# Kernel optimization log

Measured on AMD Instinct MI355X. Metric: run time of the kernel, lower is better.

Reference implementation:

```python
import jax, jax.numpy as jnp
import numpy as np

N_REV, N_USER, N_ITEM, DEG, D = 100000, 4096, 4096, 16, 64
HID = 128

def setup_inputs() -> dict:
    key = jax.random.key(0)
    ks = jax.random.split(key, 9)
    return {
        "review_vecs": jax.random.normal(ks[0], (N_REV, D), jnp.float32),
        "user_vecs": jax.random.normal(ks[1], (N_USER, D), jnp.float32),
        "item_vecs": jax.random.normal(ks[2], (N_ITEM, D), jnp.float32),
        "user_weights": jax.random.normal(ks[3], (DEG * 2 * D, HID), jnp.float32) * 0.05,
        "item_weights": jax.random.normal(ks[4], (DEG * 2 * D, HID), jnp.float32) * 0.05,
        "adj0": jax.random.randint(ks[5], (N_USER, DEG), 0, N_REV, jnp.int32),
        "adj1": jax.random.randint(ks[6], (N_USER, DEG), 0, N_ITEM, jnp.int32),
        "adj2": jax.random.randint(ks[7], (N_ITEM, DEG), 0, N_REV, jnp.int32),
        "adj3": jax.random.randint(ks[8], (N_ITEM, DEG), 0, N_USER, jnp.int32),
    }

def _sdpa(q, k, v):
    # dense scaled dot-product attention: q,k [N,d], v [N,F]
    scale = 1.0 / jnp.sqrt(jnp.asarray(q.shape[-1], q.dtype))
    w = jax.nn.softmax(jnp.einsum('nd,md->nm', q, k) * scale, axis=-1)
    return jnp.einsum('nm,mf->nf', w, v)

def reference(review_vecs, user_vecs, item_vecs, user_weights, item_weights,
              adj0, adj1, adj2, adj3):
    # dropout=0.0 -> identity; feature-dim shuffle is random augmentation,
    # replaced by identity permutation for a deterministic reference.
    ur = review_vecs[adj0]           # [Nu, deg, D]
    ri = item_vecs[adj1]             # [Nu, deg, D]
    ir = review_vecs[adj2]           # [Ni, deg, D]
    ru = user_vecs[adj3]             # [Ni, deg, D]
    cu = jnp.concatenate([ur, ri], axis=2).reshape(adj0.shape[0], -1)  # [Nu, deg*2D]
    ci = jnp.concatenate([ir, ru], axis=2).reshape(adj2.shape[0], -1)  # [Ni, deg*2D]
    cu = _sdpa(user_vecs, user_vecs, cu)
    ci = _sdpa(item_vecs, item_vecs, ci)
    user_out = jax.nn.relu(cu @ user_weights)   # [Nu, HID]
    item_out = jax.nn.relu(ci @ item_weights)   # [Ni, HID]
    return user_out, item_out
```

## Files before the change

### kernel.cpp

```cpp
#include <hip/hip_runtime.h>
#include <hip/hip_bf16.h>
#include <math.h>

#define N_NODES 4096
#define N_REV 100000
#define DEG 16
#define DIM 64
#define HID 128

typedef __attribute__((ext_vector_type(8))) short bf16x8;
typedef __attribute__((ext_vector_type(4))) float f32x4;
typedef __attribute__((ext_vector_type(16))) float f32x16;

static __device__ __forceinline__ unsigned pk2(float a, float b) {
    __hip_bfloat162 h = __float22bfloat162_rn(make_float2(a, b));
    return *reinterpret_cast<unsigned*>(&h);
}

static __device__ __forceinline__ void gl_lds16(const void* g, void* l) {
    __builtin_amdgcn_global_load_lds(
        (const __attribute__((address_space(1))) unsigned int*)g,
        (__attribute__((address_space(3))) unsigned int*)l, 16, 0, 0);
}

__global__ __launch_bounds__(256)
void prep_w(const float* __restrict__ uW, const float* __restrict__ iW,
            ushort* __restrict__ wt)
{
    __shared__ float wt_f[64 * 128];
    const int t = threadIdx.x;
    const int side = blockIdx.x >> 5, kc = blockIdx.x & 31;
    const float* __restrict__ W = side ? iW : uW;
    const float4* src = (const float4*)(W + (size_t)kc * 64 * 128);
    #pragma unroll
    for (int j = 0; j < 8; ++j)
        ((float4*)wt_f)[j * 256 + t] = src[j * 256 + t];
    __syncthreads();
    #pragma unroll
    for (int j = 0; j < 4; ++j) {
        int c = j * 256 + t;
        int h = c >> 3, seg = c & 7;
        int sp = seg ^ (h & 7);
        float v[8];
        #pragma unroll
        for (int jj = 0; jj < 8; ++jj) v[jj] = wt_f[(sp * 8 + jj) * 128 + h];
        uint4 o;
        o.x = pk2(v[0], v[1]); o.y = pk2(v[2], v[3]);
        o.z = pk2(v[4], v[5]); o.w = pk2(v[6], v[7]);
        *(uint4*)(wt + ((size_t)(side * 32 + kc) * 1024 + c) * 8) = o;
    }
}

#define GB_STRIDE 16384
#define GADJ_OFF  32768

__global__ __launch_bounds__(256)
void gemm_gather(const float* __restrict__ review,
                 const float* __restrict__ userv,
                 const float* __restrict__ itemv,
                 const ushort* __restrict__ wt,
                 const int* __restrict__ adj0, const int* __restrict__ adj1,
                 const int* __restrict__ adj2, const int* __restrict__ adj3,
                 ushort* __restrict__ vprojT,
                 ushort* __restrict__ Ub, ushort* __restrict__ Ib)
{
    const int t = threadIdx.x;
    if (blockIdx.x >= 512) {
        int i = (blockIdx.x - 512) * 256 + t;
        const float* src; ushort* dst; int j;
        if (i < 32768) { src = userv; dst = Ub; j = i; }
        else           { src = itemv; dst = Ib; j = i - 32768; }
        float4 a = ((const float4*)src)[j * 2];
        float4 b = ((const float4*)src)[j * 2 + 1];
        uint4 o;
        o.x = pk2(a.x, a.y); o.y = pk2(a.z, a.w);
        o.z = pk2(b.x, b.y); o.w = pk2(b.z, b.w);
        ((uint4*)dst)[j] = o;
        return;
    }

    const int side = blockIdx.x >> 8, rem = blockIdx.x & 255;
    const int tile = (rem & 7) | ((rem >> 4) << 3);
    const int hb   = (rem >> 3) & 1;
    const int* __restrict__ adjA = side ? adj2 : adj0;
    const int* __restrict__ adjB = side ? adj3 : adj1;
    const float* __restrict__ vecB = side ? userv : itemv;
    const ushort* __restrict__ wbase = wt + (size_t)side * 32 * 8192;
    ushort* __restrict__ outT = vprojT + (size_t)side * HID * N_NODES;

    __shared__ __align__(16) char smem[36864];
    int* adjs = (int*)(smem + GADJ_OFF);
    const int w = t >> 6, lane = t & 63;
    const int wm = w >> 1, wn = w & 1;
    const int g = lane >> 4, qi = lane & 15;
    const int swz = (qi & 7) << 4;

    if (t < 128)
        ((int4*)adjs)[t] = ((const int4*)(adjA + tile * 512))[t];
    else
        ((int4*)adjs)[t] = ((const int4*)(adjB + tile * 512))[t - 128];
    __syncthreads();

    f32x4 acc[2];
    #pragma unroll
    for (int i = 0; i < 2; ++i) acc[i] = f32x4{0.f, 0.f, 0.f, 0.f};

    auto stage = [&](int kc, int b) {
        const int d = kc >> 1, half = kc & 1;
        char* base = smem + b * GB_STRIDE;
        const float* vs = half ? vecB : review;
        #pragma unroll
        for (int j = 0; j < 2; ++j) {
            int c = j * 256 + t;
            int row = c >> 4, seg = c & 15;
            int idx = adjs[half * 512 + row * 16 + d];
            gl_lds16(vs + (size_t)idx * 64 + (seg ^ (row & 7)) * 4,
                     base + (c >> 6) * 1024);
        }
        const ushort* wsrc = wbase + (size_t)kc * 8192;
        #pragma unroll
        for (int j = 0; j < 2; ++j) {
            int c = j * 256 + t;
            gl_lds16(wsrc + (size_t)(hb * 512 + c) * 8,
                     base + 8192 + (c >> 6) * 1024);
        }
    };

    stage(0, 0);
    __syncthreads();

    for (int kc = 0; kc < 32; ++kc) {
        const int cur = kc & 1;
        if (kc < 31) stage(kc + 1, cur ^ 1);

        const char* cb = smem + cur * GB_STRIDE;
        const int ab0 = (wm * 16 + qi) * 256 + g * 32;
        f32x4 af0 = *(const f32x4*)(cb + ((ab0)       ^ swz));
        f32x4 af1 = *(const f32x4*)(cb + ((ab0 + 16)  ^ swz));
        f32x4 af2 = *(const f32x4*)(cb + ((ab0 + 128) ^ swz));
        f32x4 af3 = *(const f32x4*)(cb + ((ab0 + 144) ^ swz));
        union { unsigned u[4]; bf16x8 s; } A0, A1;
        A0.u[0] = pk2(af0[0], af0[1]); A0.u[1] = pk2(af0[2], af0[3]);
        A0.u[2] = pk2(af1[0], af1[1]); A0.u[3] = pk2(af1[2], af1[3]);
        A1.u[0] = pk2(af2[0], af2[1]); A1.u[1] = pk2(af2[2], af2[3]);
        A1.u[2] = pk2(af3[0], af3[1]); A1.u[3] = pk2(af3[2], af3[3]);

        #pragma unroll
        for (int nf = 0; nf < 2; ++nf) {
            int bbase = 8192 + (wn * 32 + nf * 16 + qi) * 128 + g * 16;
            bf16x8 b0 = *(const bf16x8*)(cb + ((bbase)      ^ swz));
            bf16x8 b1 = *(const bf16x8*)(cb + ((bbase + 64) ^ swz));
            acc[nf] = __builtin_amdgcn_mfma_f32_16x16x32_bf16(A0.s, b0, acc[nf], 0, 0, 0);
            acc[nf] = __builtin_amdgcn_mfma_f32_16x16x32_bf16(A1.s, b1, acc[nf], 0, 0, 0);
        }
        __syncthreads();
    }

    #pragma unroll
    for (int nf = 0; nf < 2; ++nf) {
        int h = hb * 64 + wn * 32 + nf * 16 + qi;
        uint2 p;
        p.x = pk2(acc[nf][0], acc[nf][1]);
        p.y = pk2(acc[nf][2], acc[nf][3]);
        *(uint2*)(outT + (size_t)h * N_NODES + tile * 32 + wm * 16 + g * 4) = p;
    }
}

#define FSTRIDE 24576
#define QSCALE 0.180336880f

__global__ __launch_bounds__(256, 2)
void flash_attn_mfma(const float* __restrict__ userv,
                     const float* __restrict__ itemv,
                     const ushort* __restrict__ Ub,
                     const ushort* __restrict__ Ib,
                     const ushort* __restrict__ vprojT,
                     ushort* __restrict__ po,
                     float* __restrict__ pl)
{
    const int grp  = blockIdx.x & 7;
    const int side = grp >> 2;
    const int qg   = grp & 3;
    const int hi   = blockIdx.x >> 3;
    const int qhi  = hi >> 3;
    const int kvb  = hi & 7;
    const int qb   = qhi * 4 + qg;
    const float* __restrict__ X = side ? itemv : userv;
    const ushort* __restrict__ Xb = side ? Ib : Ub;
    const ushort* __restrict__ V = vprojT + (size_t)side * HID * N_NODES;
    const int part = side * 8 + kvb;

    __shared__ __align__(16) char smem[49152];

    const int t = threadIdx.x;
    const int w = t >> 6, lane = t & 63;
    const int col = lane & 31, h5 = lane >> 5;
    const int q0 = qb * 128 + w * 32;

    bf16x8 qf[4];
    {
        const float* qp = X + (size_t)(q0 + col) * DIM;
        #pragma unroll
        for (int ks = 0; ks < 4; ++ks) {
            int d0 = ks * 16 + h5 * 8;
            float4 v0 = *(const float4*)(qp + d0);
            float4 v1 = *(const float4*)(qp + d0 + 4);
            union { unsigned u[4]; bf16x8 s; } rr;
            rr.u[0] = pk2(v0.x * QSCALE, v0.y * QSCALE);
            rr.u[1] = pk2(v0.z * QSCALE, v0.w * QSCALE);
            rr.u[2] = pk2(v1.x * QSCALE, v1.y * QSCALE);
            rr.u[3] = pk2(v1.z * QSCALE, v1.w * QSCALE);
            qf[ks] = rr.s;
        }
    }

    const f32x16 z16 = {0.f,0.f,0.f,0.f, 0.f,0.f,0.f,0.f,
                        0.f,0.f,0.f,0.f, 0.f,0.f,0.f,0.f};
    f32x16 o[4];
    #pragma unroll
    for (int ht = 0; ht < 4; ++ht) o[ht] = z16;
    float psum = 0.f;

    auto stage = [&](int it, int b) {
        const int k0 = kvb * 512 + it * 64;
        char* base = smem + b * FSTRIDE;
        #pragma unroll
        for (int j = 0; j < 2; ++j) {
            int c = j * 256 + t;
            int row = c >> 3, seg = c & 7;
            gl_lds16(Xb + (size_t)(k0 + row) * 64 + (seg ^ (row & 7)) * 8,
                     base + (c >> 6) * 1024);
        }
        #pragma unroll
        for (int j = 0; j < 4; ++j) {
            int c = j * 256 + t;
            int hh = c >> 3, seg = c & 7;
            gl_lds16(V + (size_t)hh * N_NODES + k0 + (seg ^ (hh & 7)) * 8,
                     base + 8192 + (c >> 6) * 1024);
        }
    };

    stage(0, 0);
    __syncthreads();

    for (int it = 0; it < 8; ++it) {
        const int cur = it & 1;
        if (it < 7) stage(it + 1, cur ^ 1);
        const char* kb = smem + cur * FSTRIDE;
        const char* vt = kb + 8192;

        #pragma unroll
        for (int T = 0; T < 2; ++T) {
            f32x16 s = z16;
            #pragma unroll
            for (int ks = 0; ks < 4; ++ks) {
                int row = T * 32 + col;
                int abase = (row * 128 + ks * 32 + h5 * 16) ^ ((row & 7) << 4);
                bf16x8 ka = *(const bf16x8*)(kb + abase);
                s = __builtin_amdgcn_mfma_f32_32x32x16_bf16(ka, qf[ks], s, 0, 0, 0);
            }
            float p[16];
            #pragma unroll
            for (int r = 0; r < 16; ++r) {
                p[r] = exp2f(s[r]);
                psum += p[r];
            }
            #pragma unroll
            for (int win = 0; win < 2; ++win) {
                unsigned ca0 = pk2(p[win*8 + 0], p[win*8 + 1]);
                unsigned ca1 = pk2(p[win*8 + 2], p[win*8 + 3]);
                unsigned cb0 = pk2(p[win*8 + 4], p[win*8 + 5]);
                unsigned cb1 = pk2(p[win*8 + 6], p[win*8 + 7]);
                asm volatile("v_permlane32_swap_b32 %0, %1"
                             : "+v"(ca0), "+v"(cb0));
                asm volatile("v_permlane32_swap_b32 %0, %1"
                             : "+v"(ca1), "+v"(cb1));
                union { unsigned u[4]; bf16x8 s8; } pa;
                pa.u[0] = ca0; pa.u[1] = ca1; pa.u[2] = cb0; pa.u[3] = cb1;
                #pragma unroll
                for (int ht = 0; ht < 4; ++ht) {
                    int hrow = ht * 32 + col;
                    int vbase = (hrow * 128 + T * 64 + win * 32 + h5 * 16)
                                ^ ((hrow & 7) << 4);
                    bf16x8 vb = *(const bf16x8*)(vt + vbase);
                    o[ht] = __builtin_amdgcn_mfma_f32_32x32x16_bf16(pa.s8, vb, o[ht], 0, 0, 0);
                }
            }
        }
        __syncthreads();
    }

    float pt = psum + __shfl_xor(psum, 32);
    if (lane < 32)
        pl[(size_t)part * N_NODES + q0 + col] = pt;

    ushort* pob = po + (size_t)part * N_NODES * HID;
    #pragma unroll
    for (int ht = 0; ht < 4; ++ht)
        #pragma unroll
        for (int r = 0; r < 16; ++r) {
            int q = q0 + (r & 3) + 8 * (r >> 2) + 4 * h5;
            pob[(size_t)q * HID + ht * 32 + col] =
                (ushort)(pk2(o[ht][r], 0.f) & 0xffffu);
        }
}

__global__ __launch_bounds__(256)
void merge_parts(const ushort* __restrict__ po, const float* __restrict__ pl,
                 float* __restrict__ out)
{
    const int grp  = blockIdx.x & 7;
    const int side = grp >> 2;
    const int qg   = grp & 3;
    const int hi   = blockIdx.x >> 3;
    const int qhi  = hi >> 3;
    const int u    = hi & 7;
    const int t = threadIdx.x;
    const int lidx = u * 256 + t;
    const int q  = (qhi * 4 + qg) * 128 + (lidx >> 4);
    const int h8 = lidx & 15;

    float s[8] = {0.f,0.f,0.f,0.f,0.f,0.f,0.f,0.f};
    float l = 0.f;
    #pragma unroll
    for (int p = 0; p < 8; ++p) {
        int part = side * 8 + p;
        uint4 v = *(const uint4*)(po + (size_t)part * (N_NODES * HID)
                                     + (size_t)q * HID + h8 * 8);
        unsigned uu[4] = {v.x, v.y, v.z, v.w};
        #pragma unroll
        for (int k = 0; k < 4; ++k) {
            union { unsigned u; float f; } lo, hi2;
            lo.u = uu[k] << 16; hi2.u = uu[k] & 0xffff0000u;
            s[k * 2]     += lo.f;
            s[k * 2 + 1] += hi2.f;
        }
        l += pl[(size_t)part * N_NODES + q];
    }
    float li = 1.0f / l;
    float4 r0, r1;
    r0.x = fmaxf(s[0] * li, 0.f); r0.y = fmaxf(s[1] * li, 0.f);
    r0.z = fmaxf(s[2] * li, 0.f); r0.w = fmaxf(s[3] * li, 0.f);
    r1.x = fmaxf(s[4] * li, 0.f); r1.y = fmaxf(s[5] * li, 0.f);
    r1.z = fmaxf(s[6] * li, 0.f); r1.w = fmaxf(s[7] * li, 0.f);
    float* op = out + ((size_t)side * N_NODES + q) * HID + h8 * 8;
    *(float4*)op = r0;
    *(float4*)(op + 4) = r1;
}

extern "C" void kernel_launch(void* const* d_in, const int* in_sizes, int n_in,
                              void* d_out, int out_size, void* d_ws, size_t ws_size,
                              hipStream_t stream)
{
    const float* review = (const float*)d_in[0];
    const float* userv  = (const float*)d_in[1];
    const float* itemv  = (const float*)d_in[2];
    const float* uW     = (const float*)d_in[3];
    const float* iW     = (const float*)d_in[4];
    const int*   adj0   = (const int*)d_in[5];
    const int*   adj1   = (const int*)d_in[6];
    const int*   adj2   = (const int*)d_in[7];
    const int*   adj3   = (const int*)d_in[8];
    float* out = (float*)d_out;

    char* ws = (char*)d_ws;
    float*  pl     = (float*)(ws + 0x000000);
    ushort* wt     = (ushort*)(ws + 0x080000);
    ushort* vprojT = (ushort*)(ws + 0x180000);
    ushort* Ub     = (ushort*)(ws + 0x380000);
    ushort* Ib     = (ushort*)(ws + 0x400000);
    ushort* po     = (ushort*)(ws + 0x480000);

    prep_w<<<64, 256, 0, stream>>>(uW, iW, wt);
    gemm_gather<<<768, 256, 0, stream>>>(review, userv, itemv, wt,
                                         adj0, adj1, adj2, adj3, vprojT,
                                         Ub, Ib);
    flash_attn_mfma<<<512, 256, 0, stream>>>(userv, itemv, Ub, Ib, vprojT,
                                             po, pl);
    merge_parts<<<512, 256, 0, stream>>>(po, pl, out);
}
```

Baseline: 56.45 us.

## Fuse all four stages into one cooperative persistent kernel with grid syncs

Replaces the four separate launches (weight prep, gather-GEMM, flash attention, merge) with a single cooperative kernel of 256 blocks of 512 threads. Each block runs two 256-thread units and separates the stages with grid-wide barriers. The aim is to remove per-launch overhead and inter-kernel gaps. In exchange it adds grid sync cost, requires 96KB LDS per block with two blocks per CU, and runs the weight prep and bf16 conversion on only some blocks while the rest idle. It falls back to the old launches if the cooperative launch fails.

```diff
diff --git a/kernel.cpp b/kernel.cpp
--- a/kernel.cpp
+++ b/kernel.cpp
@@ -1,6 +1,9 @@
 #include <hip/hip_runtime.h>
 #include <hip/hip_bf16.h>
+#include <hip/hip_cooperative_groups.h>
 #include <math.h>
+
+namespace cg = cooperative_groups;
 
 #define N_NODES 4096
 #define N_REV 100000
@@ -23,63 +26,22 @@
         (__attribute__((address_space(3))) unsigned int*)l, 16, 0, 0);
 }
 
-__global__ __launch_bounds__(256)
-void prep_w(const float* __restrict__ uW, const float* __restrict__ iW,
-            ushort* __restrict__ wt)
-{
-    __shared__ float wt_f[64 * 128];
-    const int t = threadIdx.x;
-    const int side = blockIdx.x >> 5, kc = blockIdx.x & 31;
-    const float* __restrict__ W = side ? iW : uW;
-    const float4* src = (const float4*)(W + (size_t)kc * 64 * 128);
-    #pragma unroll
-    for (int j = 0; j < 8; ++j)
-        ((float4*)wt_f)[j * 256 + t] = src[j * 256 + t];
-    __syncthreads();
-    #pragma unroll
-    for (int j = 0; j < 4; ++j) {
-        int c = j * 256 + t;
-        int h = c >> 3, seg = c & 7;
-        int sp = seg ^ (h & 7);
-        float v[8];
-        #pragma unroll
-        for (int jj = 0; jj < 8; ++jj) v[jj] = wt_f[(sp * 8 + jj) * 128 + h];
-        uint4 o;
-        o.x = pk2(v[0], v[1]); o.y = pk2(v[2], v[3]);
-        o.z = pk2(v[4], v[5]); o.w = pk2(v[6], v[7]);
-        *(uint4*)(wt + ((size_t)(side * 32 + kc) * 1024 + c) * 8) = o;
-    }
-}
-
 #define GB_STRIDE 16384
 #define GADJ_OFF  32768
-
-__global__ __launch_bounds__(256)
-void gemm_gather(const float* __restrict__ review,
-                 const float* __restrict__ userv,
-                 const float* __restrict__ itemv,
-                 const ushort* __restrict__ wt,
-                 const int* __restrict__ adj0, const int* __restrict__ adj1,
-                 const int* __restrict__ adj2, const int* __restrict__ adj3,
-                 ushort* __restrict__ vprojT,
-                 ushort* __restrict__ Ub, ushort* __restrict__ Ib)
-{
-    const int t = threadIdx.x;
-    if (blockIdx.x >= 512) {
-        int i = (blockIdx.x - 512) * 256 + t;
-        const float* src; ushort* dst; int j;
-        if (i < 32768) { src = userv; dst = Ub; j = i; }
-        else           { src = itemv; dst = Ib; j = i - 32768; }
-        float4 a = ((const float4*)src)[j * 2];
-        float4 b = ((const float4*)src)[j * 2 + 1];
-        uint4 o;
-        o.x = pk2(a.x, a.y); o.y = pk2(a.z, a.w);
-        o.z = pk2(b.x, b.y); o.w = pk2(b.z, b.w);
-        ((uint4*)dst)[j] = o;
-        return;
-    }
-
-    const int side = blockIdx.x >> 8, rem = blockIdx.x & 255;
+#define FSTRIDE   24576
+#define QSCALE    0.180336880f
+
+static __device__ __forceinline__
+void gemm_unit(char* U, int tl, int unit,
+               const float* __restrict__ review,
+               const float* __restrict__ userv,
+               const float* __restrict__ itemv,
+               const ushort* __restrict__ wt,
+               const int* __restrict__ adj0, const int* __restrict__ adj1,
+               const int* __restrict__ adj2, const int* __restrict__ adj3,
+               ushort* __restrict__ vprojT)
+{
+    const int side = unit >> 8, rem = unit & 255;
     const int tile = (rem & 7) | ((rem >> 4) << 3);
     const int hb   = (rem >> 3) & 1;
     const int* __restrict__ adjA = side ? adj2 : adj0;
@@ -88,17 +50,16 @@
     const ushort* __restrict__ wbase = wt + (size_t)side * 32 * 8192;
     ushort* __restrict__ outT = vprojT + (size_t)side * HID * N_NODES;
 
-    __shared__ __align__(16) char smem[36864];
-    int* adjs = (int*)(smem + GADJ_OFF);
-    const int w = t >> 6, lane = t & 63;
+    int* adjs = (int*)(U + GADJ_OFF);
+    const int w = tl >> 6, lane = tl & 63;
     const int wm = w >> 1, wn = w & 1;
     const int g = lane >> 4, qi = lane & 15;
     const int swz = (qi & 7) << 4;
 
-    if (t < 128)
-        ((int4*)adjs)[t] = ((const int4*)(adjA + tile * 512))[t];
+    if (tl < 128)
+        ((int4*)adjs)[tl] = ((const int4*)(adjA + tile * 512))[tl];
     else
-        ((int4*)adjs)[t] = ((const int4*)(adjB + tile * 512))[t - 128];
+        ((int4*)adjs)[tl] = ((const int4*)(adjB + tile * 512))[tl - 128];
     __syncthreads();
 
     f32x4 acc[2];
@@ -107,11 +68,11 @@
 
     auto stage = [&](int kc, int b) {
         const int d = kc >> 1, half = kc & 1;
-        char* base = smem + b * GB_STRIDE;
+        char* base = U + b * GB_STRIDE;
         const float* vs = half ? vecB : review;
         #pragma unroll
         for (int j = 0; j < 2; ++j) {
-            int c = j * 256 + t;
+            int c = j * 256 + tl;
             int row = c >> 4, seg = c & 15;
             int idx = adjs[half * 512 + row * 16 + d];
             gl_lds16(vs + (size_t)idx * 64 + (seg ^ (row & 7)) * 4,
@@ -120,7 +81,7 @@
         const ushort* wsrc = wbase + (size_t)kc * 8192;
         #pragma unroll
         for (int j = 0; j < 2; ++j) {
-            int c = j * 256 + t;
+            int c = j * 256 + tl;
             gl_lds16(wsrc + (size_t)(hb * 512 + c) * 8,
                      base + 8192 + (c >> 6) * 1024);
         }
@@ -133,7 +94,7 @@
         const int cur = kc & 1;
         if (kc < 31) stage(kc + 1, cur ^ 1);
 
-        const char* cb = smem + cur * GB_STRIDE;
+        const char* cb = U + cur * GB_STRIDE;
         const int ab0 = (wm * 16 + qi) * 256 + g * 32;
         f32x4 af0 = *(const f32x4*)(cb + ((ab0)       ^ swz));
         f32x4 af1 = *(const f32x4*)(cb + ((ab0 + 16)  ^ swz));
@@ -166,22 +127,19 @@
     }
 }
 
-#define FSTRIDE 24576
-#define QSCALE 0.180336880f
-
-__global__ __launch_bounds__(256, 2)
-void flash_attn_mfma(const float* __restrict__ userv,
-                     const float* __restrict__ itemv,
-                     const ushort* __restrict__ Ub,
-                     const ushort* __restrict__ Ib,
-                     const ushort* __restrict__ vprojT,
-                     ushort* __restrict__ po,
-                     float* __restrict__ pl)
-{
-    const int grp  = blockIdx.x & 7;
+static __device__ __forceinline__
+void flash_unit(char* U, int tl, int unit,
+                const float* __restrict__ userv,
+                const float* __restrict__ itemv,
+                const ushort* __restrict__ Ub,
+                const ushort* __restrict__ Ib,
+                const ushort* __restrict__ vprojT,
+                ushort* __restrict__ po, float* __restrict__ pl)
+{
+    const int grp  = unit & 7;
     const int side = grp >> 2;
     const int qg   = grp & 3;
-    const int hi   = blockIdx.x >> 3;
+    const int hi   = unit >> 3;
     const int qhi  = hi >> 3;
     const int kvb  = hi & 7;
     const int qb   = qhi * 4 + qg;
@@ -190,10 +148,7 @@
     const ushort* __restrict__ V = vprojT + (size_t)side * HID * N_NODES;
     const int part = side * 8 + kvb;
 
-    __shared__ __align__(16) char smem[49152];
-
-    const int t = threadIdx.x;
-    const int w = t >> 6, lane = t & 63;
+    const int w = tl >> 6, lane = tl & 63;
     const int col = lane & 31, h5 = lane >> 5;
     const int q0 = qb * 128 + w * 32;
 
@@ -223,17 +178,17 @@
 
     auto stage = [&](int it, int b) {
         const int k0 = kvb * 512 + it * 64;
-        char* base = smem + b * FSTRIDE;
+        char* base = U + b * FSTRIDE;
         #pragma unroll
         for (int j = 0; j < 2; ++j) {
-            int c = j * 256 + t;
+            int c = j * 256 + tl;
             int row = c >> 3, seg = c & 7;
             gl_lds16(Xb + (size_t)(k0 + row) * 64 + (seg ^ (row & 7)) * 8,
                      base + (c >> 6) * 1024);
         }
         #pragma unroll
         for (int j = 0; j < 4; ++j) {
-            int c = j * 256 + t;
+            int c = j * 256 + tl;
             int hh = c >> 3, seg = c & 7;
             gl_lds16(V + (size_t)hh * N_NODES + k0 + (seg ^ (hh & 7)) * 8,
                      base + 8192 + (c >> 6) * 1024);
@@ -246,7 +201,7 @@
     for (int it = 0; it < 8; ++it) {
         const int cur = it & 1;
         if (it < 7) stage(it + 1, cur ^ 1);
-        const char* kb = smem + cur * FSTRIDE;
+        const char* kb = U + cur * FSTRIDE;
         const char* vt = kb + 8192;
 
         #pragma unroll
@@ -305,18 +260,18 @@
         }
 }
 
-__global__ __launch_bounds__(256)
-void merge_parts(const ushort* __restrict__ po, const float* __restrict__ pl,
-                 float* __restrict__ out)
-{
-    const int grp  = blockIdx.x & 7;
+static __device__ __forceinline__
+void merge_unit(int tl, int unit,
+                const ushort* __restrict__ po, const float* __restrict__ pl,
+                float* __restrict__ out)
+{
+    const int grp  = unit & 7;
     const int side = grp >> 2;
     const int qg   = grp & 3;
-    const int hi   = blockIdx.x >> 3;
+    const int hi   = unit >> 3;
     const int qhi  = hi >> 3;
     const int u    = hi & 7;
-    const int t = threadIdx.x;
-    const int lidx = u * 256 + t;
+    const int lidx = u * 256 + tl;
     const int q  = (qhi * 4 + qg) * 128 + (lidx >> 4);
     const int h8 = lidx & 15;
 
@@ -346,6 +301,153 @@
     float* op = out + ((size_t)side * N_NODES + q) * HID + h8 * 8;
     *(float4*)op = r0;
     *(float4*)(op + 4) = r1;
+}
+
+__global__ __launch_bounds__(512, 2)
+void fused_all(const float* __restrict__ review,
+               const float* __restrict__ userv,
+               const float* __restrict__ itemv,
+               const float* __restrict__ uW,
+               const float* __restrict__ iW,
+               const int* __restrict__ adj0, const int* __restrict__ adj1,
+               const int* __restrict__ adj2, const int* __restrict__ adj3,
+               ushort* __restrict__ wt,
+               ushort* __restrict__ vprojT,
+               ushort* __restrict__ Ub, ushort* __restrict__ Ib,
+               ushort* __restrict__ po, float* __restrict__ pl,
+               float* __restrict__ out)
+{
+    __shared__ __align__(16) char smem[98304];
+    const int t = threadIdx.x;
+    const int blk = blockIdx.x;
+    const int uh = t >> 8;
+    const int tl = t & 255;
+    const int unit = blk * 2 + uh;
+
+    if (blk < 128) {
+        int i = blk * 512 + t;
+        const float* src; ushort* dst; int j;
+        if (i < 32768) { src = userv; dst = Ub; j = i; }
+        else           { src = itemv; dst = Ib; j = i - 32768; }
+        float4 a = ((const float4*)src)[j * 2];
+        float4 b = ((const float4*)src)[j * 2 + 1];
+        uint4 o;
+        o.x = pk2(a.x, a.y); o.y = pk2(a.z, a.w);
+        o.z = pk2(b.x, b.y); o.w = pk2(b.z, b.w);
+        ((uint4*)dst)[j] = o;
+    } else if (blk < 192) {
+        float* wt_f = (float*)smem;
+        const int b = blk - 128;
+        const int side = b >> 5, kc = b & 31;
+        const float* __restrict__ W = side ? iW : uW;
+        const float4* src = (const float4*)(W + (size_t)kc * 64 * 128);
+        #pragma unroll
+        for (int j = 0; j < 4; ++j)
+            ((float4*)wt_f)[j * 512 + t] = src[j * 512 + t];
+        __syncthreads();
+        #pragma unroll
+        for (int j = 0; j < 2; ++j) {
+            int c = j * 512 + t;
+            int h = c >> 3, seg = c & 7;
+            int sp = seg ^ (h & 7);
+            float v[8];
+            #pragma unroll
+            for (int jj = 0; jj < 8; ++jj) v[jj] = wt_f[(sp * 8 + jj) * 128 + h];
+            uint4 o;
+            o.x = pk2(v[0], v[1]); o.y = pk2(v[2], v[3]);
+            o.z = pk2(v[4], v[5]); o.w = pk2(v[6], v[7]);
+            *(uint4*)(wt + ((size_t)(side * 32 + kc) * 1024 + c) * 8) = o;
+        }
+    }
+    cg::this_grid().sync();
+
+    gemm_unit(smem + uh * 36864, tl, unit, review, userv, itemv, wt,
+              adj0, adj1, adj2, adj3, vprojT);
+    cg::this_grid().sync();
+
+    flash_unit(smem + uh * 49152, tl, unit, userv, itemv, Ub, Ib, vprojT,
+               po, pl);
+    cg::this_grid().sync();
+
+    merge_unit(tl, unit, po, pl, out);
+}
+
+__global__ __launch_bounds__(256)
+void prep_w(const float* __restrict__ uW, const float* __restrict__ iW,
+            ushort* __restrict__ wt)
+{
+    __shared__ float wt_f[64 * 128];
+    const int t = threadIdx.x;
+    const int side = blockIdx.x >> 5, kc = blockIdx.x & 31;
+    const float* __restrict__ W = side ? iW : uW;
+    const float4* src = (const float4*)(W + (size_t)kc * 64 * 128);
+    #pragma unroll
+    for (int j = 0; j < 8; ++j)
+        ((float4*)wt_f)[j * 256 + t] = src[j * 256 + t];
+    __syncthreads();
+    #pragma unroll
+    for (int j = 0; j < 4; ++j) {
+        int c = j * 256 + t;
+        int h = c >> 3, seg = c & 7;
+        int sp = seg ^ (h & 7);
+        float v[8];
+        #pragma unroll
+        for (int jj = 0; jj < 8; ++jj) v[jj] = wt_f[(sp * 8 + jj) * 128 + h];
+        uint4 o;
+        o.x = pk2(v[0], v[1]); o.y = pk2(v[2], v[3]);
+        o.z = pk2(v[4], v[5]); o.w = pk2(v[6], v[7]);
+        *(uint4*)(wt + ((size_t)(side * 32 + kc) * 1024 + c) * 8) = o;
+    }
+}
+
+__global__ __launch_bounds__(256)
+void gemm_gather(const float* __restrict__ review,
+                 const float* __restrict__ userv,
+                 const float* __restrict__ itemv,
+                 const ushort* __restrict__ wt,
+                 const int* __restrict__ adj0, const int* __restrict__ adj1,
+                 const int* __restrict__ adj2, const int* __restrict__ adj3,
+                 ushort* __restrict__ vprojT,
+                 ushort* __restrict__ Ub, ushort* __restrict__ Ib)
+{
+    const int t = threadIdx.x;
+    if (blockIdx.x >= 512) {
+        int i = (blockIdx.x - 512) * 256 + t;
+        const float* src; ushort* dst; int j;
+        if (i < 32768) { src = userv; dst = Ub; j = i; }
+        else           { src = itemv; dst = Ib; j = i - 32768; }
+        float4 a = ((const float4*)src)[j * 2];
+        float4 b = ((const float4*)src)[j * 2 + 1];
+        uint4 o;
+        o.x = pk2(a.x, a.y); o.y = pk2(a.z, a.w);
+        o.z = pk2(b.x, b.y); o.w = pk2(b.z, b.w);
+        ((uint4*)dst)[j] = o;
+        return;
+    }
+    __shared__ __align__(16) char smem[36864];
+    gemm_unit(smem, t, blockIdx.x, review, userv, itemv, wt,
+              adj0, adj1, adj2, adj3, vprojT);
+}
+
+__global__ __launch_bounds__(256, 2)
+void flash_attn_mfma(const float* __restrict__ userv,
+                     const float* __restrict__ itemv,
+                     const ushort* __restrict__ Ub,
+                     const ushort* __restrict__ Ib,
+                     const ushort* __restrict__ vprojT,
+                     ushort* __restrict__ po,
+                     float* __restrict__ pl)
+{
+    __shared__ __align__(16) char smem[49152];
+    flash_unit(smem, threadIdx.x, blockIdx.x, userv, itemv, Ub, Ib, vprojT,
+               po, pl);
+}
+
+__global__ __launch_bounds__(256)
+void merge_parts(const ushort* __restrict__ po, const float* __restrict__ pl,
+                 float* __restrict__ out)
+{
+    merge_unit(threadIdx.x, blockIdx.x, po, pl, out);
 }
 
 extern "C" void kernel_launch(void* const* d_in, const int* in_sizes, int n_in,
@@ -371,11 +473,33 @@
     ushort* Ib     = (ushort*)(ws + 0x400000);
     ushort* po     = (ushort*)(ws + 0x480000);
 
-    prep_w<<<64, 256, 0, stream>>>(uW, iW, wt);
-    gemm_gather<<<768, 256, 0, stream>>>(review, userv, itemv, wt,
-                                         adj0, adj1, adj2, adj3, vprojT,
-                                         Ub, Ib);
-    flash_attn_mfma<<<512, 256, 0, stream>>>(userv, itemv, Ub, Ib, vprojT,
-                                             po, pl);
-    merge_parts<<<512, 256, 0, stream>>>(po, pl, out);
-}
+    int dev = 0;
+    hipGetDevice(&dev);
+    int coop = 0;
+    hipDeviceGetAttribute(&coop, hipDeviceAttributeCooperativeLaunch, dev);
+    int nb = 0;
+    if (coop)
+        hipOccupancyMaxActiveBlocksPerMultiprocessor(
+            &nb, (const void*)fused_all, 512, 0);
+
+    hipError_t err = hipErrorUnknown;
+    if (coop && nb >= 1) {
+        void* args[] = {
+            (void*)&review, (void*)&userv, (void*)&itemv, (void*)&uW,
+            (void*)&iW, (void*)&adj0, (void*)&adj1, (void*)&adj2,
+            (void*)&adj3, (void*)&wt, (void*)&vprojT, (void*)&Ub,
+            (void*)&Ib, (void*)&po, (void*)&pl, (void*)&out
+        };
+        err = hipLaunchCooperativeKernel((const void*)fused_all, dim3(256),
+                                         dim3(512), args, 0, stream);
+    }
+    if (err != hipSuccess) {
+        prep_w<<<64, 256, 0, stream>>>(uW, iW, wt);
+        gemm_gather<<<768, 256, 0, stream>>>(review, userv, itemv, wt,
+                                             adj0, adj1, adj2, adj3, vprojT,
+                                             Ub, Ib);
+        flash_attn_mfma<<<512, 256, 0, stream>>>(userv, itemv, Ub, Ib,
+                                                 vprojT, po, pl);
+        merge_parts<<<512, 256, 0, stream>>>(po, pl, out);
+    }
+}
```

New measurement: 56.29 us. No clear change (-0.3%).

## Pre-swizzle K and V into MFMA fragment layout and drop LDS staging in attention

Applied to the files above, without the earlier changes.

The producer kernels now write the bf16 key matrix and the projected value matrix directly in per-lane MFMA fragment order. The attention kernel then reads its fragments with coalesced 16-byte global loads instead of double-buffered global-to-LDS staging with barriers. Because it no longer needs shared memory, the attention launch bound is raised to four blocks per SM, and block-to-work mapping is reordered so the 16 partitions of a query block are adjacent. This removes LDS traffic and synchronization, but every wave now re-reads K and V from L2 with no on-chip sharing across waves, and latency hiding depends on occupancy rather than explicit prefetch.

```diff
diff --git a/kernel.cpp b/kernel.cpp
--- a/kernel.cpp
+++ b/kernel.cpp
@@ -61,21 +61,23 @@
                  const ushort* __restrict__ wt,
                  const int* __restrict__ adj0, const int* __restrict__ adj1,
                  const int* __restrict__ adj2, const int* __restrict__ adj3,
-                 ushort* __restrict__ vprojT,
-                 ushort* __restrict__ Ub, ushort* __restrict__ Ib)
+                 ushort* __restrict__ Vf,
+                 ushort* __restrict__ Kf)
 {
     const int t = threadIdx.x;
     if (blockIdx.x >= 512) {
-        int i = (blockIdx.x - 512) * 256 + t;
-        const float* src; ushort* dst; int j;
-        if (i < 32768) { src = userv; dst = Ub; j = i; }
-        else           { src = itemv; dst = Ib; j = i - 32768; }
-        float4 a = ((const float4*)src)[j * 2];
-        float4 b = ((const float4*)src)[j * 2 + 1];
+        int id = (blockIdx.x - 512) * 256 + t;
+        int lane = id & 63, ks = (id >> 6) & 3, kt = (id >> 8) & 127;
+        int side = id >> 15;
+        const float* X = side ? itemv : userv;
+        const float* src = X + (size_t)(kt * 32 + (lane & 31)) * DIM
+                             + ks * 16 + (lane >> 5) * 8;
+        float4 a = *(const float4*)src;
+        float4 b = *(const float4*)(src + 4);
         uint4 o;
         o.x = pk2(a.x, a.y); o.y = pk2(a.z, a.w);
         o.z = pk2(b.x, b.y); o.w = pk2(b.z, b.w);
-        ((uint4*)dst)[j] = o;
+        ((uint4*)Kf)[id] = o;
         return;
     }
 
@@ -86,7 +88,6 @@
     const int* __restrict__ adjB = side ? adj3 : adj1;
     const float* __restrict__ vecB = side ? userv : itemv;
     const ushort* __restrict__ wbase = wt + (size_t)side * 32 * 8192;
-    ushort* __restrict__ outT = vprojT + (size_t)side * HID * N_NODES;
 
     __shared__ __align__(16) char smem[36864];
     int* adjs = (int*)(smem + GADJ_OFF);
@@ -156,41 +157,40 @@
         __syncthreads();
     }
 
+    ushort* VfS = Vf + (size_t)side * 524288;
+    const int ht_ = hb * 2 + wn;
+    const int kw  = tile * 2 + wm;
+    const int lv  = 32 * (g >> 1);
     #pragma unroll
     for (int nf = 0; nf < 2; ++nf) {
-        int h = hb * 64 + wn * 32 + nf * 16 + qi;
+        int colv = nf * 16 + qi;
         uint2 p;
         p.x = pk2(acc[nf][0], acc[nf][1]);
         p.y = pk2(acc[nf][2], acc[nf][3]);
-        *(uint2*)(outT + (size_t)h * N_NODES + tile * 32 + wm * 16 + g * 4) = p;
-    }
-}
-
-#define FSTRIDE 24576
+        char* dst = (char*)(VfS + (((size_t)(kw * 4 + ht_)) * 64 + colv + lv) * 8)
+                    + (g & 1) * 8;
+        *(uint2*)dst = p;
+    }
+}
+
 #define QSCALE 0.180336880f
 
-__global__ __launch_bounds__(256, 2)
+__global__ __launch_bounds__(256, 4)
 void flash_attn_mfma(const float* __restrict__ userv,
                      const float* __restrict__ itemv,
-                     const ushort* __restrict__ Ub,
-                     const ushort* __restrict__ Ib,
-                     const ushort* __restrict__ vprojT,
+                     const ushort* __restrict__ Kf,
+                     const ushort* __restrict__ Vf,
                      ushort* __restrict__ po,
                      float* __restrict__ pl)
 {
-    const int grp  = blockIdx.x & 7;
-    const int side = grp >> 2;
-    const int qg   = grp & 3;
-    const int hi   = blockIdx.x >> 3;
-    const int qhi  = hi >> 3;
-    const int kvb  = hi & 7;
-    const int qb   = qhi * 4 + qg;
+    const int grp  = blockIdx.x & 15;
+    const int side = grp >> 3;
+    const int kvb  = grp & 7;
+    const int qb   = blockIdx.x >> 4;
     const float* __restrict__ X = side ? itemv : userv;
-    const ushort* __restrict__ Xb = side ? Ib : Ub;
-    const ushort* __restrict__ V = vprojT + (size_t)side * HID * N_NODES;
+    const ushort* __restrict__ KfS = Kf + (size_t)side * 262144;
+    const ushort* __restrict__ VfS = Vf + (size_t)side * 524288;
     const int part = side * 8 + kvb;
-
-    __shared__ __align__(16) char smem[49152];
 
     const int t = threadIdx.x;
     const int w = t >> 6, lane = t & 63;
@@ -221,73 +221,44 @@
     for (int ht = 0; ht < 4; ++ht) o[ht] = z16;
     float psum = 0.f;
 
-    auto stage = [&](int it, int b) {
-        const int k0 = kvb * 512 + it * 64;
-        char* base = smem + b * FSTRIDE;
-        #pragma unroll
-        for (int j = 0; j < 2; ++j) {
-            int c = j * 256 + t;
-            int row = c >> 3, seg = c & 7;
-            gl_lds16(Xb + (size_t)(k0 + row) * 64 + (seg ^ (row & 7)) * 8,
-                     base + (c >> 6) * 1024);
-        }
-        #pragma unroll
-        for (int j = 0; j < 4; ++j) {
-            int c = j * 256 + t;
-            int hh = c >> 3, seg = c & 7;
-            gl_lds16(V + (size_t)hh * N_NODES + k0 + (seg ^ (hh & 7)) * 8,
-                     base + 8192 + (c >> 6) * 1024);
-        }
-    };
-
-    stage(0, 0);
-    __syncthreads();
-
-    for (int it = 0; it < 8; ++it) {
-        const int cur = it & 1;
-        if (it < 7) stage(it + 1, cur ^ 1);
-        const char* kb = smem + cur * FSTRIDE;
-        const char* vt = kb + 8192;
-
-        #pragma unroll
-        for (int T = 0; T < 2; ++T) {
-            f32x16 s = z16;
+    for (int kt8 = 0; kt8 < 16; ++kt8) {
+        const int kt = kvb * 16 + kt8;
+
+        bf16x8 ka[4];
+        #pragma unroll
+        for (int ks = 0; ks < 4; ++ks)
+            ka[ks] = *(const bf16x8*)(KfS + (size_t)((kt * 4 + ks) * 64 + lane) * 8);
+        f32x16 s = z16;
+        #pragma unroll
+        for (int ks = 0; ks < 4; ++ks)
+            s = __builtin_amdgcn_mfma_f32_32x32x16_bf16(ka[ks], qf[ks], s, 0, 0, 0);
+
+        float p[16];
+        #pragma unroll
+        for (int r = 0; r < 16; ++r) {
+            p[r] = exp2f(s[r]);
+            psum += p[r];
+        }
+
+        #pragma unroll
+        for (int win = 0; win < 2; ++win) {
+            unsigned ca0 = pk2(p[win*8 + 0], p[win*8 + 1]);
+            unsigned ca1 = pk2(p[win*8 + 2], p[win*8 + 3]);
+            unsigned cb0 = pk2(p[win*8 + 4], p[win*8 + 5]);
+            unsigned cb1 = pk2(p[win*8 + 6], p[win*8 + 7]);
+            asm volatile("v_permlane32_swap_b32 %0, %1"
+                         : "+v"(ca0), "+v"(cb0));
+            asm volatile("v_permlane32_swap_b32 %0, %1"
+                         : "+v"(ca1), "+v"(cb1));
+            union { unsigned u[4]; bf16x8 s8; } pa;
+            pa.u[0] = ca0; pa.u[1] = ca1; pa.u[2] = cb0; pa.u[3] = cb1;
+            const int kw = kt * 2 + win;
             #pragma unroll
-            for (int ks = 0; ks < 4; ++ks) {
-                int row = T * 32 + col;
-                int abase = (row * 128 + ks * 32 + h5 * 16) ^ ((row & 7) << 4);
-                bf16x8 ka = *(const bf16x8*)(kb + abase);
-                s = __builtin_amdgcn_mfma_f32_32x32x16_bf16(ka, qf[ks], s, 0, 0, 0);
+            for (int ht = 0; ht < 4; ++ht) {
+                bf16x8 vb = *(const bf16x8*)(VfS + (size_t)((kw * 4 + ht) * 64 + lane) * 8);
+                o[ht] = __builtin_amdgcn_mfma_f32_32x32x16_bf16(pa.s8, vb, o[ht], 0, 0, 0);
             }
-            float p[16];
-            #pragma unroll
-            for (int r = 0; r < 16; ++r) {
-                p[r] = exp2f(s[r]);
-                psum += p[r];
-            }
-            #pragma unroll
-            for (int win = 0; win < 2; ++win) {
-                unsigned ca0 = pk2(p[win*8 + 0], p[win*8 + 1]);
-                unsigned ca1 = pk2(p[win*8 + 2], p[win*8 + 3]);
-                unsigned cb0 = pk2(p[win*8 + 4], p[win*8 + 5]);
-                unsigned cb1 = pk2(p[win*8 + 6], p[win*8 + 7]);
-                asm volatile("v_permlane32_swap_b32 %0, %1"
-                             : "+v"(ca0), "+v"(cb0));
-                asm volatile("v_permlane32_swap_b32 %0, %1"
-                             : "+v"(ca1), "+v"(cb1));
-                union { unsigned u[4]; bf16x8 s8; } pa;
-                pa.u[0] = ca0; pa.u[1] = ca1; pa.u[2] = cb0; pa.u[3] = cb1;
-                #pragma unroll
-                for (int ht = 0; ht < 4; ++ht) {
-                    int hrow = ht * 32 + col;
-                    int vbase = (hrow * 128 + T * 64 + win * 32 + h5 * 16)
-                                ^ ((hrow & 7) << 4);
-                    bf16x8 vb = *(const bf16x8*)(vt + vbase);
-                    o[ht] = __builtin_amdgcn_mfma_f32_32x32x16_bf16(pa.s8, vb, o[ht], 0, 0, 0);
-                }
-            }
-        }
-        __syncthreads();
+        }
     }
 
     float pt = psum + __shfl_xor(psum, 32);
@@ -364,18 +335,15 @@
     float* out = (float*)d_out;
 
     char* ws = (char*)d_ws;
-    float*  pl     = (float*)(ws + 0x000000);
-    ushort* wt     = (ushort*)(ws + 0x080000);
-    ushort* vprojT = (ushort*)(ws + 0x180000);
-    ushort* Ub     = (ushort*)(ws + 0x380000);
-    ushort* Ib     = (ushort*)(ws + 0x400000);
-    ushort* po     = (ushort*)(ws + 0x480000);
+    float*  pl = (float*)(ws + 0x000000);
+    ushort* wt = (ushort*)(ws + 0x080000);
+    ushort* Vf = (ushort*)(ws + 0x180000);
+    ushort* Kf = (ushort*)(ws + 0x380000);
+    ushort* po = (ushort*)(ws + 0x480000);
 
     prep_w<<<64, 256, 0, stream>>>(uW, iW, wt);
     gemm_gather<<<768, 256, 0, stream>>>(review, userv, itemv, wt,
-                                         adj0, adj1, adj2, adj3, vprojT,
-                                         Ub, Ib);
-    flash_attn_mfma<<<512, 256, 0, stream>>>(userv, itemv, Ub, Ib, vprojT,
-                                             po, pl);
+                                         adj0, adj1, adj2, adj3, Vf, Kf);
+    flash_attn_mfma<<<512, 256, 0, stream>>>(userv, itemv, Kf, Vf, po, pl);
     merge_parts<<<512, 256, 0, stream>>>(po, pl, out);
 }
```

New measurement: 88.10 us. 1.56x slower.
